# Optimization experiments

Measured on AMD Instinct MI355X. Metric: run time of the kernel, lower is better.

The kernel has to match this reference:

```python
import jax, jax.numpy as jnp
import numpy as np

N_FLOWS = 20
DIM = 4
BATCH = 8388608  # 2**23 samples -> 128 MB fp32 input


def setup_inputs() -> dict:
    key = jax.random.key(0)
    k1, k2, k3, k4 = jax.random.split(key, 4)
    return {
        "X": jax.random.normal(k1, (BATCH, DIM), dtype=jnp.float32),
        "x0s": jax.random.normal(k2, (N_FLOWS, DIM), dtype=jnp.float32),
        "alpha_primes": jax.random.normal(k3, (N_FLOWS,), dtype=jnp.float32),
        "beta_primes": jax.random.normal(k4, (N_FLOWS,), dtype=jnp.float32),
    }


def reference(X, x0s, alpha_primes, beta_primes):
    """Chain of 20 pyro-style Radial flow transforms on dim-4 vectors.

    Each flow: alpha = softplus(alpha'), beta = -alpha + softplus(beta')
               y = x + beta * (x - x0) / (alpha + ||x - x0||)
    """
    def step(x, params):
        x0, a_p, b_p = params
        alpha = jax.nn.softplus(a_p)                 # scalar > 0
        beta = -alpha + jax.nn.softplus(b_p)         # beta >= -alpha (invertibility)
        diff = x - x0                                # [B, 4]
        r = jnp.linalg.norm(diff, axis=-1, keepdims=True)  # [B, 1]
        return x + beta * diff / (alpha + r), None

    X, _ = jax.lax.scan(step, X, (x0s, alpha_primes, beta_primes))
    return X
```

## Files before the change

### kernel.cpp

```cpp
#include <hip/hip_runtime.h>

#define N_FLOWS 20
#define DIM 4
#define ITEMS 8
#define BLOCK 256

__global__ __launch_bounds__(BLOCK) void radial_flow_kernel(
    const float* __restrict__ X,
    const float* __restrict__ x0s,
    const float* __restrict__ alpha_primes,
    const float* __restrict__ beta_primes,
    float* __restrict__ out,
    int batch)
{
    const float4* __restrict__ Xv = (const float4*)X;
    const float4* __restrict__ x0v = (const float4*)x0s;
    float4* __restrict__ Ov = (float4*)out;

    const long base = (long)blockIdx.x * (BLOCK * ITEMS) + threadIdx.x;

    float4 x[ITEMS];
    bool ok[ITEMS];
#pragma unroll
    for (int i = 0; i < ITEMS; ++i) {
        long idx = base + (long)i * BLOCK;
        ok[i] = idx < batch;
        if (ok[i]) x[i] = Xv[idx];
    }

#pragma unroll
    for (int f = 0; f < N_FLOWS; ++f) {
        float alpha = __logf(1.0f + __expf(alpha_primes[f]));
        float beta  = __logf(1.0f + __expf(beta_primes[f])) - alpha;
        float4 c = x0v[f];
#pragma unroll
        for (int i = 0; i < ITEMS; ++i) {
            float dx = x[i].x - c.x;
            float dy = x[i].y - c.y;
            float dz = x[i].z - c.z;
            float dw = x[i].w - c.w;
            float r2 = dx * dx;
            r2 = __builtin_fmaf(dy, dy, r2);
            r2 = __builtin_fmaf(dz, dz, r2);
            r2 = __builtin_fmaf(dw, dw, r2);
            float r = __builtin_amdgcn_sqrtf(r2);
            float t = beta * __builtin_amdgcn_rcpf(alpha + r);
            x[i].x = __builtin_fmaf(t, dx, x[i].x);
            x[i].y = __builtin_fmaf(t, dy, x[i].y);
            x[i].z = __builtin_fmaf(t, dz, x[i].z);
            x[i].w = __builtin_fmaf(t, dw, x[i].w);
        }
    }

#pragma unroll
    for (int i = 0; i < ITEMS; ++i) {
        long idx = base + (long)i * BLOCK;
        if (ok[i]) Ov[idx] = x[i];
    }
}

extern "C" void kernel_launch(void* const* d_in, const int* in_sizes, int n_in,
                              void* d_out, int out_size, void* d_ws, size_t ws_size,
                              hipStream_t stream) {
    const float* X   = (const float*)d_in[0];
    const float* x0s = (const float*)d_in[1];
    const float* ap  = (const float*)d_in[2];
    const float* bp  = (const float*)d_in[3];
    float* out = (float*)d_out;

    int batch = in_sizes[0] / DIM;
    int blocks = (batch + BLOCK * ITEMS - 1) / (BLOCK * ITEMS);
    radial_flow_kernel<<<blocks, BLOCK, 0, stream>>>(X, x0s, ap, bp, out, batch);
}
```

Baseline: 249.5 us.

## Precompute flow params in setup kernel, use packed v2f math, split tail

A one-thread-per-flow setup kernel now computes the softplus alpha/beta values once and stores them with x0 in a packed workspace table. The main kernel reads that table instead of evaluating exp/log per thread, uses 2-wide float vectors so the compiler can emit packed FP32 ops, and drops bounds checks for full tiles. Leftover rows go to a separate tail kernel. The cost is two extra launches and a workspace round trip. The kernel is likely memory-bound, so the ALU savings may not show.

```diff
diff --git a/kernel.cpp b/kernel.cpp
--- a/kernel.cpp
+++ b/kernel.cpp
@@ -5,58 +5,92 @@
 #define ITEMS 8
 #define BLOCK 256
 
-__global__ __launch_bounds__(BLOCK) void radial_flow_kernel(
-    const float* __restrict__ X,
-    const float* __restrict__ x0s,
-    const float* __restrict__ alpha_primes,
-    const float* __restrict__ beta_primes,
-    float* __restrict__ out,
-    int batch)
+typedef float v2f __attribute__((ext_vector_type(2)));
+
+__global__ void radial_setup(const float* __restrict__ x0s,
+                             const float* __restrict__ alpha_primes,
+                             const float* __restrict__ beta_primes,
+                             float* __restrict__ ws) {
+    int f = threadIdx.x;
+    if (f < N_FLOWS) {
+        float alpha = __logf(1.0f + __expf(alpha_primes[f]));
+        float beta  = __logf(1.0f + __expf(beta_primes[f])) - alpha;
+        float* p = ws + 8 * f;
+        p[0] = x0s[4 * f + 0];
+        p[1] = x0s[4 * f + 1];
+        p[2] = x0s[4 * f + 2];
+        p[3] = x0s[4 * f + 3];
+        p[4] = alpha;
+        p[5] = beta;
+        p[6] = 0.0f;
+        p[7] = 0.0f;
+    }
+}
+
+__global__ __launch_bounds__(BLOCK) void radial_main(
+    const float4* __restrict__ Xv,
+    const float4* __restrict__ P,
+    float4* __restrict__ Ov)
 {
-    const float4* __restrict__ Xv = (const float4*)X;
-    const float4* __restrict__ x0v = (const float4*)x0s;
-    float4* __restrict__ Ov = (float4*)out;
+    const unsigned base = blockIdx.x * (BLOCK * ITEMS) + threadIdx.x;
 
-    const long base = (long)blockIdx.x * (BLOCK * ITEMS) + threadIdx.x;
-
-    float4 x[ITEMS];
-    bool ok[ITEMS];
+    v2f a[ITEMS], b[ITEMS];
 #pragma unroll
     for (int i = 0; i < ITEMS; ++i) {
-        long idx = base + (long)i * BLOCK;
-        ok[i] = idx < batch;
-        if (ok[i]) x[i] = Xv[idx];
+        float4 v = Xv[base + i * BLOCK];
+        a[i] = (v2f){v.x, v.y};
+        b[i] = (v2f){v.z, v.w};
     }
 
 #pragma unroll
     for (int f = 0; f < N_FLOWS; ++f) {
-        float alpha = __logf(1.0f + __expf(alpha_primes[f]));
-        float beta  = __logf(1.0f + __expf(beta_primes[f])) - alpha;
-        float4 c = x0v[f];
+        float4 c  = P[2 * f];
+        float4 ab = P[2 * f + 1];
+        v2f c01 = (v2f){c.x, c.y};
+        v2f c23 = (v2f){c.z, c.w};
+        float alpha = ab.x, beta = ab.y;
 #pragma unroll
         for (int i = 0; i < ITEMS; ++i) {
-            float dx = x[i].x - c.x;
-            float dy = x[i].y - c.y;
-            float dz = x[i].z - c.z;
-            float dw = x[i].w - c.w;
-            float r2 = dx * dx;
-            r2 = __builtin_fmaf(dy, dy, r2);
-            r2 = __builtin_fmaf(dz, dz, r2);
-            r2 = __builtin_fmaf(dw, dw, r2);
-            float r = __builtin_amdgcn_sqrtf(r2);
-            float t = beta * __builtin_amdgcn_rcpf(alpha + r);
-            x[i].x = __builtin_fmaf(t, dx, x[i].x);
-            x[i].y = __builtin_fmaf(t, dy, x[i].y);
-            x[i].z = __builtin_fmaf(t, dz, x[i].z);
-            x[i].w = __builtin_fmaf(t, dw, x[i].w);
+            v2f da = a[i] - c01;
+            v2f db = b[i] - c23;
+            v2f q  = da * da;
+            q += db * db;
+            float r2 = q.x + q.y;
+            float r  = __builtin_amdgcn_sqrtf(r2);
+            float t  = beta * __builtin_amdgcn_rcpf(alpha + r);
+            v2f tv = (v2f){t, t};
+            a[i] = tv * da + a[i];
+            b[i] = tv * db + b[i];
         }
     }
 
 #pragma unroll
     for (int i = 0; i < ITEMS; ++i) {
-        long idx = base + (long)i * BLOCK;
-        if (ok[i]) Ov[idx] = x[i];
+        float4 v;
+        v.x = a[i].x; v.y = a[i].y; v.z = b[i].x; v.w = b[i].y;
+        Ov[base + i * BLOCK] = v;
     }
+}
+
+__global__ void radial_tail(const float4* __restrict__ Xv,
+                            const float4* __restrict__ P,
+                            float4* __restrict__ Ov,
+                            int start, int batch)
+{
+    int idx = start + blockIdx.x * blockDim.x + threadIdx.x;
+    if (idx >= batch) return;
+    float4 v = Xv[idx];
+#pragma unroll
+    for (int f = 0; f < N_FLOWS; ++f) {
+        float4 c  = P[2 * f];
+        float4 ab = P[2 * f + 1];
+        float dx = v.x - c.x, dy = v.y - c.y, dz = v.z - c.z, dw = v.w - c.w;
+        float r2 = dx * dx + dy * dy + dz * dz + dw * dw;
+        float r  = __builtin_amdgcn_sqrtf(r2);
+        float t  = ab.y * __builtin_amdgcn_rcpf(ab.x + r);
+        v.x += t * dx; v.y += t * dy; v.z += t * dz; v.w += t * dw;
+    }
+    Ov[idx] = v;
 }
 
 extern "C" void kernel_launch(void* const* d_in, const int* in_sizes, int n_in,
@@ -67,8 +101,21 @@
     const float* ap  = (const float*)d_in[2];
     const float* bp  = (const float*)d_in[3];
     float* out = (float*)d_out;
+    float* ws  = (float*)d_ws;
 
     int batch = in_sizes[0] / DIM;
-    int blocks = (batch + BLOCK * ITEMS - 1) / (BLOCK * ITEMS);
-    radial_flow_kernel<<<blocks, BLOCK, 0, stream>>>(X, x0s, ap, bp, out, batch);
+
+    radial_setup<<<1, 64, 0, stream>>>(x0s, ap, bp, ws);
+
+    const int tile = BLOCK * ITEMS;
+    int full_blocks = batch / tile;
+    if (full_blocks > 0)
+        radial_main<<<full_blocks, BLOCK, 0, stream>>>(
+            (const float4*)X, (const float4*)ws, (float4*)out);
+
+    int done = full_blocks * tile;
+    int rem = batch - done;
+    if (rem > 0)
+        radial_tail<<<(rem + 255) / 256, 256, 0, stream>>>(
+            (const float4*)X, (const float4*)ws, (float4*)out, done, batch);
 }
```

New measurement: 244.0 us. 2.2% less time.
